# Optimization experiments

Measured on AMD Instinct MI355X. Metric: run time of the kernel, lower is better.

Reference implementation:

```python
import jax, jax.numpy as jnp
import numpy as np


def _pack_ternary(codes):
    # codes: [N, K] uint8 in {0,1,2} (encoded = ternary_value + 1)
    N, K = codes.shape
    c = codes.reshape(N, K // 4, 4).astype(np.uint8)
    shifts = np.array([0, 2, 4, 6], dtype=np.uint8)
    packed = (c << shifts).sum(axis=-1).astype(np.uint8)
    return packed  # [N, K//4]


def setup_inputs() -> dict:
    key = jax.random.key(0)
    k1, k2 = jax.random.split(key)
    M, K, N = 8192, 4096, 4096
    x = jax.random.normal(k1, (M, K), dtype=jnp.float16)
    # valid INT2 packed ternary weights: 2-bit fields in {0,1,2} = value+1
    codes = np.asarray(jax.random.randint(k2, (N, K), 0, 3), dtype=np.uint8)
    W_packed = jnp.asarray(_pack_ternary(codes), dtype=jnp.uint8)
    gamma = jnp.ones((1,), dtype=jnp.float32)
    return {"x": x, "W_packed": W_packed, "gamma": gamma}


def _unpack_w(W_packed, K):
    # W_packed: [N, K//4] uint8 -> ternary float32 W: [N, K]
    N = W_packed.shape[0]
    shifts = jnp.array([0, 2, 4, 6], dtype=jnp.uint8)
    fields = (W_packed[:, :, None] >> shifts) & jnp.uint8(3)  # [N, K//4, 4]
    w = fields.reshape(N, -1)[:, :K].astype(jnp.float32) - 1.0  # {-1,0,1}
    return w


def reference(x, W_packed, gamma):
    K = x.shape[-1]
    W = _unpack_w(W_packed, K)  # [N, K] ternary
    # Y = X @ W.T * gamma (kernel does fp16 TC GEMM with inline dequant scale)
    Xf = x.astype(jnp.float32)
    Y = jnp.einsum('mk,nk->mn', Xf, W) * gamma[0]
    return Y.astype(jnp.float16)
```

## Files before the change

### kernel.cpp

```cpp
#include <hip/hip_runtime.h>
#include <cstdint>
#include <cstddef>

#define M_DIM 8192
#define N_DIM 4096
#define K_DIM 4096

typedef _Float16 f16x8 __attribute__((ext_vector_type(8)));
typedef float f32x4 __attribute__((ext_vector_type(4)));
typedef unsigned short ushort8 __attribute__((ext_vector_type(8)));

#define GLOAD_LDS16(g, l)                                                      \
  __builtin_amdgcn_global_load_lds(                                            \
      (const __attribute__((address_space(1))) void*)(g),                      \
      (__attribute__((address_space(3))) void*)(l), 16, 0, 0)

__device__ inline uint32_t lutf16(uint32_t c) {
  return (c == 1u) ? 0u : (0x3C00u | ((uint32_t)(c == 0u) << 15));
}

__global__ __launch_bounds__(256) void prep_x(const float4* __restrict__ X,
                                              ushort8* __restrict__ Xf) {
  int i = blockIdx.x * 256 + threadIdx.x;
  float4 f0 = X[2 * (size_t)i], f1 = X[2 * (size_t)i + 1];
  ushort8 us;
  us[0] = __builtin_bit_cast(uint16_t, (_Float16)f0.x);
  us[1] = __builtin_bit_cast(uint16_t, (_Float16)f0.y);
  us[2] = __builtin_bit_cast(uint16_t, (_Float16)f0.z);
  us[3] = __builtin_bit_cast(uint16_t, (_Float16)f0.w);
  us[4] = __builtin_bit_cast(uint16_t, (_Float16)f1.x);
  us[5] = __builtin_bit_cast(uint16_t, (_Float16)f1.y);
  us[6] = __builtin_bit_cast(uint16_t, (_Float16)f1.z);
  us[7] = __builtin_bit_cast(uint16_t, (_Float16)f1.w);
  Xf[i] = us;
}

__global__ __launch_bounds__(256) void prep_w(const uint2* __restrict__ W,
                                              uint4* __restrict__ Wf) {
  int i = blockIdx.x * 256 + threadIdx.x;
  uint2 wv = W[(size_t)i];
  uint32_t x = wv.x & 0xFFu, y = wv.y & 0xFFu;
  uint4 o;
  o.x = lutf16(x & 3u) | (lutf16((x >> 2) & 3u) << 16);
  o.y = lutf16((x >> 4) & 3u) | (lutf16((x >> 6) & 3u) << 16);
  o.z = lutf16(y & 3u) | (lutf16((y >> 2) & 3u) << 16);
  o.w = lutf16((y >> 4) & 3u) | (lutf16((y >> 6) & 3u) << 16);
  Wf[i] = o;
}

__global__ __launch_bounds__(512, 2) void gemm8(
    const _Float16* __restrict__ A,
    const _Float16* __restrict__ B,
    const float* __restrict__ G,
    float* __restrict__ C) {
  __shared__ __align__(16) _Float16 As[2][16384];
  __shared__ __align__(16) _Float16 Bs[2][16384];

  const int tid = threadIdx.x;
  const int wid = tid >> 6;
  const int lane = tid & 63;
  const int wr = wid >> 2;
  const int wcq = wid & 3;
  const int fr = lane & 15, kg = lane >> 4;

  int bid = (int)blockIdx.x;
  int swz = ((bid & 7) << 6) | (bid >> 3);
  const int bm = (swz >> 4) * 256;
  const int bn = (swz & 15) * 256;

  const int sr8 = lane >> 3;
  const int scol = ((lane & 7) ^ sr8) * 8;

  f32x4 acc[8][4] = {};
  f16x8 bfr[4][2];
  f16x8 afr[2][2];

#define STAGE(t, ht)                                                           \
  do {                                                                         \
    const int buf_ = (t) & 1;                                                  \
    const int kt_ = (t) << 6;                                                  \
    const _Float16* src_ =                                                     \
        ((ht) < 2) ? (B + (size_t)bn * K_DIM) : (A + (size_t)bm * K_DIM);      \
    _Float16* dst_ = ((ht) < 2) ? Bs[buf_] : As[buf_];                         \
    const int h_ = (ht) & 1;                                                   \
    _Pragma("unroll") for (int j_ = 0; j_ < 2; ++j_) {                         \
      int sg_ = h_ * 16 + wid * 2 + j_;                                        \
      int row_ = sg_ * 8 + sr8;                                                \
      GLOAD_LDS16(src_ + (size_t)row_ * K_DIM + kt_ + scol, dst_ + sg_ * 512); \
    }                                                                          \
  } while (0)

#define READ_B(t)                                                              \
  do {                                                                         \
    const int buf_ = (t) & 1;                                                  \
    _Pragma("unroll") for (int ni_ = 0; ni_ < 4; ++ni_)                        \
        _Pragma("unroll") for (int ks_ = 0; ks_ < 2; ++ks_) {                  \
      int row_ = wcq * 64 + ni_ * 16 + fr;                                     \
      bfr[ni_][ks_] = *reinterpret_cast<const f16x8*>(                         \
          Bs[buf_] + row_ * 64 + (((ks_ * 4 + kg) ^ (row_ & 7)) * 8));         \
    }                                                                          \
  } while (0)

#define READ_A(t, q)                                                           \
  do {                                                                         \
    const int buf_ = (t) & 1;                                                  \
    _Pragma("unroll") for (int m2_ = 0; m2_ < 2; ++m2_)                        \
        _Pragma("unroll") for (int ks_ = 0; ks_ < 2; ++ks_) {                  \
      int row_ = wr * 128 + ((q) * 2 + m2_) * 16 + fr;                         \
      afr[m2_][ks_] = *reinterpret_cast<const f16x8*>(                         \
          As[buf_] + row_ * 64 + (((ks_ * 4 + kg) ^ (row_ & 7)) * 8));         \
    }                                                                          \
  } while (0)

#define MFMA_Q(q)                                                              \
  do {                                                                         \
    __builtin_amdgcn_s_setprio(1);                                             \
    _Pragma("unroll") for (int m2_ = 0; m2_ < 2; ++m2_)                        \
        _Pragma("unroll") for (int ni_ = 0; ni_ < 4; ++ni_)                    \
            _Pragma("unroll") for (int ks_ = 0; ks_ < 2; ++ks_)                \
                acc[(q) * 2 + m2_][ni_] =                                      \
        __builtin_amdgcn_mfma_f32_16x16x32_f16(                                \
            afr[m2_][ks_], bfr[ni_][ks_], acc[(q) * 2 + m2_][ni_], 0, 0, 0);   \
    __builtin_amdgcn_s_setprio(0);                                             \
  } while (0)

#define END_SYNC() __builtin_amdgcn_s_barrier()
#define VM6() asm volatile("s_waitcnt vmcnt(6)" ::: "memory")
#define VM0() asm volatile("s_waitcnt vmcnt(0)" ::: "memory")

  STAGE(0, 0); STAGE(0, 1); STAGE(0, 2); STAGE(0, 3);
  STAGE(1, 0); STAGE(1, 1); STAGE(1, 2);
  VM6();
  END_SYNC();

  for (int i = 0; i < 31; ++i) {
    const int t = 2 * i;
    READ_B(t); READ_A(t, 0); STAGE(t + 1, 3);
    MFMA_Q(0); END_SYNC();
    READ_A(t, 1); STAGE(t + 2, 0);
    MFMA_Q(1); END_SYNC();
    READ_A(t, 2); STAGE(t + 2, 1);
    MFMA_Q(2); END_SYNC();
    READ_A(t, 3); STAGE(t + 2, 2); VM6();
    MFMA_Q(3); END_SYNC();
    READ_B(t + 1); READ_A(t + 1, 0); STAGE(t + 2, 3);
    MFMA_Q(0); END_SYNC();
    READ_A(t + 1, 1); STAGE(t + 3, 0);
    MFMA_Q(1); END_SYNC();
    READ_A(t + 1, 2); STAGE(t + 3, 1);
    MFMA_Q(2); END_SYNC();
    READ_A(t + 1, 3); STAGE(t + 3, 2); VM6();
    MFMA_Q(3); END_SYNC();
  }
  {
    const int t = 62;
    READ_B(t); READ_A(t, 0); STAGE(t + 1, 3);
    MFMA_Q(0); END_SYNC();
    READ_A(t, 1); MFMA_Q(1); END_SYNC();
    READ_A(t, 2); MFMA_Q(2); END_SYNC();
    READ_A(t, 3); VM0(); MFMA_Q(3); END_SYNC();
    READ_B(t + 1); READ_A(t + 1, 0); MFMA_Q(0); END_SYNC();
    READ_A(t + 1, 1); MFMA_Q(1); END_SYNC();
    READ_A(t + 1, 2); MFMA_Q(2); END_SYNC();
    READ_A(t + 1, 3); MFMA_Q(3); END_SYNC();
  }

  float g = G[0];
  if (!(__builtin_fabsf(g) >= 0.001f && __builtin_fabsf(g) <= 1000.0f)) g = 1.0f;
#pragma unroll
  for (int m = 0; m < 8; ++m)
#pragma unroll
    for (int ni = 0; ni < 4; ++ni) {
      int col = bn + wcq * 64 + ni * 16 + fr;
      int row0 = bm + wr * 128 + m * 16 + kg * 4;
#pragma unroll
      for (int j = 0; j < 4; ++j)
        C[(size_t)(row0 + j) * N_DIM + col] = acc[m][ni][j] * g;
    }
#undef STAGE
#undef READ_B
#undef READ_A
#undef MFMA_Q
#undef END_SYNC
#undef VM6
#undef VM0
}

__global__ __launch_bounds__(256) void gemm_inline(
    const float* __restrict__ X, const uint32_t* __restrict__ W,
    const float* __restrict__ G, float* __restrict__ C) {
  __shared__ __align__(16) _Float16 As[128 * 64];
  __shared__ __align__(16) _Float16 Bs[128 * 64];

  const int tid = threadIdx.x;
  const int wave = tid >> 6;
  const int lane = tid & 63;
  const int wr = wave >> 1, wc = wave & 1;
  const int fr = lane & 15, kg = lane >> 4;
  const int bm = blockIdx.y * 128, bn = blockIdx.x * 128;
  const int brow = tid >> 1, bhalf = tid & 1;

  f32x4 acc[4][4] = {};

  for (int kt = 0; kt < K_DIM; kt += 64) {
#pragma unroll
    for (int i = 0; i < 4; ++i) {
      int c = i * 256 + tid;
      int row = c >> 3, cc = c & 7;
      const float4* p =
          (const float4*)(X + (size_t)(bm + row) * K_DIM + kt + cc * 8);
      float4 f0 = p[0], f1 = p[1];
      ushort8 us;
      us[0] = __builtin_bit_cast(uint16_t, (_Float16)f0.x);
      us[1] = __builtin_bit_cast(uint16_t, (_Float16)f0.y);
      us[2] = __builtin_bit_cast(uint16_t, (_Float16)f0.z);
      us[3] = __builtin_bit_cast(uint16_t, (_Float16)f0.w);
      us[4] = __builtin_bit_cast(uint16_t, (_Float16)f1.x);
      us[5] = __builtin_bit_cast(uint16_t, (_Float16)f1.y);
      us[6] = __builtin_bit_cast(uint16_t, (_Float16)f1.z);
      us[7] = __builtin_bit_cast(uint16_t, (_Float16)f1.w);
      *reinterpret_cast<ushort8*>((uint16_t*)As + row * 64 +
                                  (cc ^ (row & 7)) * 8) = us;
    }
    {
      const uint32_t* wp =
          W + (size_t)(bn + brow) * 1024 + (kt >> 2) + bhalf * 8;
      uint32_t w[8];
      *(uint4*)(w) = *(const uint4*)(wp);
      *(uint4*)(w + 4) = *(const uint4*)(wp + 4);
#pragma unroll
      for (int q = 0; q < 4; ++q) {
        uint32_t x = w[2 * q] & 0xFFu, y = w[2 * q + 1] & 0xFFu;
        uint4 o;
        o.x = lutf16(x & 3u) | (lutf16((x >> 2) & 3u) << 16);
        o.y = lutf16((x >> 4) & 3u) | (lutf16((x >> 6) & 3u) << 16);
        o.z = lutf16(y & 3u) | (lutf16((y >> 2) & 3u) << 16);
        o.w = lutf16((y >> 4) & 3u) | (lutf16((y >> 6) & 3u) << 16);
        int slot = (bhalf * 4 + q) ^ (brow & 7);
        *reinterpret_cast<uint4*>((uint16_t*)Bs + brow * 64 + slot * 8) = o;
      }
    }
    __syncthreads();

#pragma unroll
    for (int ks = 0; ks < 2; ++ks) {
      f16x8 a[4], b[4];
#pragma unroll
      for (int r = 0; r < 4; ++r) {
        int row = wr * 64 + r * 16 + fr;
        a[r] = *reinterpret_cast<const f16x8*>(
            As + row * 64 + ((ks * 4 + kg) ^ (row & 7)) * 8);
      }
#pragma unroll
      for (int c = 0; c < 4; ++c) {
        int row = wc * 64 + c * 16 + fr;
        b[c] = *reinterpret_cast<const f16x8*>(
            Bs + row * 64 + ((ks * 4 + kg) ^ (row & 7)) * 8);
      }
#pragma unroll
      for (int r = 0; r < 4; ++r)
#pragma unroll
        for (int c = 0; c < 4; ++c)
          acc[r][c] = __builtin_amdgcn_mfma_f32_16x16x32_f16(a[r], b[c],
                                                             acc[r][c], 0, 0, 0);
    }
    __syncthreads();
  }

  float g = G[0];
  if (!(__builtin_fabsf(g) >= 0.001f && __builtin_fabsf(g) <= 1000.0f)) g = 1.0f;
#pragma unroll
  for (int r = 0; r < 4; ++r)
#pragma unroll
    for (int c = 0; c < 4; ++c) {
      int col = bn + wc * 64 + c * 16 + fr;
      int row0 = bm + wr * 64 + r * 16 + kg * 4;
#pragma unroll
      for (int j = 0; j < 4; ++j)
        C[(size_t)(row0 + j) * N_DIM + col] = acc[r][c][j] * g;
    }
}

extern "C" void kernel_launch(void* const* d_in, const int* in_sizes, int n_in,
                              void* d_out, int out_size, void* d_ws,
                              size_t ws_size, hipStream_t stream) {
  const float* x = (const float*)d_in[0];
  const uint32_t* w32 = (const uint32_t*)d_in[1];
  const float* gamma = (const float*)d_in[2];
  float* out = (float*)d_out;
  (void)in_sizes; (void)n_in; (void)out_size;

  const size_t xf_bytes = (size_t)M_DIM * K_DIM * 2;
  const size_t wf_bytes = (size_t)N_DIM * K_DIM * 2;

  if (ws_size >= xf_bytes + wf_bytes) {
    _Float16* xf = (_Float16*)d_ws;
    _Float16* wf = (_Float16*)((char*)d_ws + xf_bytes);
    prep_x<<<M_DIM * K_DIM / 8 / 256, 256, 0, stream>>>((const float4*)x,
                                                        (ushort8*)xf);
    prep_w<<<N_DIM * K_DIM / 8 / 256, 256, 0, stream>>>((const uint2*)w32,
                                                        (uint4*)wf);
    gemm8<<<(M_DIM / 256) * (N_DIM / 256), 512, 0, stream>>>(xf, wf, gamma,
                                                             out);
  } else {
    dim3 grid(N_DIM / 128, M_DIM / 128);
    gemm_inline<<<grid, 256, 0, stream>>>(x, w32, gamma, out);
  }
}
```

Measured before the change: 295.6 us.

## Replace interleaved quarter-step pipeline with simple per-tile double-buffered loop

Replaces the hand-interleaved schedule with a plain double-buffered loop. The old schedule split each k-tile's staging into four pieces, put them between the MFMA quarters, and used a barrier plus a partial vmcnt(6) wait after each quarter. The new loop waits vmcnt(0) and hits one barrier per k-tile, then issues the whole next tile's global-to-LDS copy and runs all four MFMA quarters. This cuts barrier count and simplifies the code. In exchange it drains all outstanding loads every tile, which may expose memory latency the finer interleave was hiding.

```diff
diff --git a/kernel.cpp b/kernel.cpp
--- a/kernel.cpp
+++ b/kernel.cpp
@@ -90,6 +90,9 @@
     }                                                                          \
   } while (0)
 
+#define STAGE_FULL(t)                                                          \
+  do { STAGE(t, 0); STAGE(t, 1); STAGE(t, 2); STAGE(t, 3); } while (0)
+
 #define READ_B(t)                                                              \
   do {                                                                         \
     const int buf_ = (t) & 1;                                                  \
@@ -124,46 +127,26 @@
     __builtin_amdgcn_s_setprio(0);                                             \
   } while (0)
 
-#define END_SYNC() __builtin_amdgcn_s_barrier()
-#define VM6() asm volatile("s_waitcnt vmcnt(6)" ::: "memory")
 #define VM0() asm volatile("s_waitcnt vmcnt(0)" ::: "memory")
 
-  STAGE(0, 0); STAGE(0, 1); STAGE(0, 2); STAGE(0, 3);
-  STAGE(1, 0); STAGE(1, 1); STAGE(1, 2);
-  VM6();
-  END_SYNC();
-
-  for (int i = 0; i < 31; ++i) {
-    const int t = 2 * i;
-    READ_B(t); READ_A(t, 0); STAGE(t + 1, 3);
-    MFMA_Q(0); END_SYNC();
-    READ_A(t, 1); STAGE(t + 2, 0);
-    MFMA_Q(1); END_SYNC();
-    READ_A(t, 2); STAGE(t + 2, 1);
-    MFMA_Q(2); END_SYNC();
-    READ_A(t, 3); STAGE(t + 2, 2); VM6();
-    MFMA_Q(3); END_SYNC();
-    READ_B(t + 1); READ_A(t + 1, 0); STAGE(t + 2, 3);
-    MFMA_Q(0); END_SYNC();
-    READ_A(t + 1, 1); STAGE(t + 3, 0);
-    MFMA_Q(1); END_SYNC();
-    READ_A(t + 1, 2); STAGE(t + 3, 1);
-    MFMA_Q(2); END_SYNC();
-    READ_A(t + 1, 3); STAGE(t + 3, 2); VM6();
-    MFMA_Q(3); END_SYNC();
+  STAGE_FULL(0);
+  for (int t = 0; t < 63; ++t) {
+    VM0();
+    __builtin_amdgcn_s_barrier();
+    STAGE_FULL(t + 1);
+    READ_B(t);
+    READ_A(t, 0); MFMA_Q(0);
+    READ_A(t, 1); MFMA_Q(1);
+    READ_A(t, 2); MFMA_Q(2);
+    READ_A(t, 3); MFMA_Q(3);
   }
-  {
-    const int t = 62;
-    READ_B(t); READ_A(t, 0); STAGE(t + 1, 3);
-    MFMA_Q(0); END_SYNC();
-    READ_A(t, 1); MFMA_Q(1); END_SYNC();
-    READ_A(t, 2); MFMA_Q(2); END_SYNC();
-    READ_A(t, 3); VM0(); MFMA_Q(3); END_SYNC();
-    READ_B(t + 1); READ_A(t + 1, 0); MFMA_Q(0); END_SYNC();
-    READ_A(t + 1, 1); MFMA_Q(1); END_SYNC();
-    READ_A(t + 1, 2); MFMA_Q(2); END_SYNC();
-    READ_A(t + 1, 3); MFMA_Q(3); END_SYNC();
-  }
+  VM0();
+  __builtin_amdgcn_s_barrier();
+  READ_B(63);
+  READ_A(63, 0); MFMA_Q(0);
+  READ_A(63, 1); MFMA_Q(1);
+  READ_A(63, 2); MFMA_Q(2);
+  READ_A(63, 3); MFMA_Q(3);
 
   float g = G[0];
   if (!(__builtin_fabsf(g) >= 0.001f && __builtin_fabsf(g) <= 1000.0f)) g = 1.0f;
@@ -178,11 +161,10 @@
         C[(size_t)(row0 + j) * N_DIM + col] = acc[m][ni][j] * g;
     }
 #undef STAGE
+#undef STAGE_FULL
 #undef READ_B
 #undef READ_A
 #undef MFMA_Q
-#undef END_SYNC
-#undef VM6
 #undef VM0
 }
 
```

Measured after the change: 304.1 us. 2.9% more time.
